# Performance work log

Measured on AMD Instinct MI355X. Metric: run time of the kernel, lower is better.

## Reference

```python
import math
import jax
import jax.numpy as jnp
import numpy as np

IMAGE_SIZE = 256
FOV_DEG = 60.0
NEAR, FAR = 0.01, 10.0
CHUNK = 128          # faces processed per scan step (bounds peak memory)
BIG_Z = 1e10         # 'infinite' depth for empty pixels


def _projection_matrix():
    f = 1.0 / math.tan(math.radians(FOV_DEG) / 2)
    return jnp.array([
        [f, 0.0, 0.0, 0.0],
        [0.0, f, 0.0, 0.0],
        [0.0, 0.0, (FAR + NEAR) / (NEAR - FAR), 2.0 * FAR * NEAR / (NEAR - FAR)],
        [0.0, 0.0, -1.0, 0.0],
    ], dtype=jnp.float32)


def _rasterize_mask(v_ndc, faces):
    """Coverage mask via edge-function triangle rasterization with a z-buffer.
    v_ndc: [V,3] ndc coords, faces: [F,3] int. Returns float [H,W] mask."""
    H = W = IMAGE_SIZE
    dt = v_ndc.dtype
    px = ((jnp.arange(W, dtype=dt) + 0.5) / W * 2.0 - 1.0)[None, None, :]  # [1,1,W]
    py = ((jnp.arange(H, dtype=dt) + 0.5) / H * 2.0 - 1.0)[None, :, None]  # [1,H,1]
    fchunks = faces.reshape(-1, CHUNK, 3)

    def body(carry, fc):
        zbuf, mask = carry
        tri = v_ndc[fc]  # [C,3,3]
        x0 = tri[:, 0, 0][:, None, None]; y0 = tri[:, 0, 1][:, None, None]; z0 = tri[:, 0, 2][:, None, None]
        x1 = tri[:, 1, 0][:, None, None]; y1 = tri[:, 1, 1][:, None, None]; z1 = tri[:, 1, 2][:, None, None]
        x2 = tri[:, 2, 0][:, None, None]; y2 = tri[:, 2, 1][:, None, None]; z2 = tri[:, 2, 2][:, None, None]
        # edge functions, [C,H,W]
        e0 = (x1 - x0) * (py - y0) - (y1 - y0) * (px - x0)
        e1 = (x2 - x1) * (py - y1) - (y2 - y1) * (px - x1)
        e2 = (x0 - x2) * (py - y2) - (y0 - y2) * (px - x2)
        inside = ((e0 >= 0) & (e1 >= 0) & (e2 >= 0)) | ((e0 <= 0) & (e1 <= 0) & (e2 <= 0))
        area = e0 + e1 + e2
        denom = jnp.where(jnp.abs(area) > 1e-12, area, 1.0)
        # barycentric-interpolated depth
        z = (e1 * z0 + e2 * z1 + e0 * z2) / denom
        zc = jnp.where(inside, z, BIG_Z)
        zbuf = jnp.minimum(zbuf, jnp.min(zc, axis=0))
        mask = jnp.maximum(mask, jnp.max(inside.astype(dt), axis=0))
        return (zbuf, mask), None

    zbuf0 = jnp.full((H, W), BIG_Z, dtype=dt)
    mask0 = jnp.zeros((H, W), dtype=dt)
    (_, mask), _ = jax.lax.scan(body, (zbuf0, mask0), fchunks)
    return mask


def setup_inputs() -> dict:
    key = jax.random.key(0)
    k1, k2, k3, k4 = jax.random.split(key, 4)
    B, V, F = 2, 4096, 4096
    verts = jax.random.normal(k1, (B, V, 3), dtype=jnp.float32)
    faces = jax.random.randint(k2, (B, F, 3), 0, V, dtype=jnp.int64 if jax.config.jax_enable_x64 else jnp.int32)
    R = jax.random.normal(k3, (B, 3, 3), dtype=jnp.float32)
    T = jax.random.normal(k4, (B, 3), dtype=jnp.float32)
    return {"verts": verts, "faces": faces, "R": R, "T": T}


def reference(verts, faces, R, T):
    proj = _projection_matrix()
    # world2cam: [R^T | -R^T t] with homogeneous bottom row, built batched
    Rt = jnp.swapaxes(R, -1, -2)                       # [B,3,3]
    t = -jnp.einsum('bij,bj->bi', Rt, T)               # [B,3]
    top = jnp.concatenate([Rt, t[..., None]], axis=-1)  # [B,3,4]
    bottom = jnp.broadcast_to(jnp.array([[0.0, 0.0, 0.0, 1.0]], dtype=verts.dtype), (R.shape[0], 1, 4))
    w2c = jnp.concatenate([top, bottom], axis=1)       # [B,4,4]
    VP = jnp.einsum('ij,bjk->bik', proj, w2c)          # [B,4,4]
    homo = jnp.concatenate([verts, jnp.ones_like(verts[..., :1])], axis=-1)  # [B,V,4]
    cam = jnp.einsum('bvk,bjk->bvj', homo, VP)         # verts_homo @ VP.T
    ndc = cam[..., :3] / jnp.maximum(cam[..., 3:], 1e-8)  # clamp(min=1e-8)
    mask = jax.vmap(_rasterize_mask)(ndc, faces)       # [B,H,W]
    return jnp.repeat(mask[..., None], 3, axis=-1)     # [B,H,W,3]
```

## Files before the change

kernel.cpp:

```cpp
#include <hip/hip_runtime.h>


#pragma clang fp contract(off)

#define HW      256
#define BATCH   2
#define VCOUNT  4096
#define FCOUNT  4096


__global__ __launch_bounds__(256)
void face_pack_kernel(const float* __restrict__ verts,
                      const int* __restrict__ faces,
                      const float* __restrict__ R,
                      const float* __restrict__ T,
                      float4* __restrict__ fpack)
{
#pragma clang fp contract(off)
    int gid = blockIdx.x * blockDim.x + threadIdx.x;
    if (gid >= BATCH * FCOUNT) return;
    int b = gid / FCOUNT;

    const float fproj = 1.7320508075688772f;

    const float* Rb = R + b * 9;
    const float* Tb = T + b * 3;

    float t0 = -((Rb[0*3+0]*Tb[0] + Rb[1*3+0]*Tb[1]) + Rb[2*3+0]*Tb[2]);
    float t1 = -((Rb[0*3+1]*Tb[0] + Rb[1*3+1]*Tb[1]) + Rb[2*3+1]*Tb[2]);
    float t2 = -((Rb[0*3+2]*Tb[0] + Rb[1*3+2]*Tb[1]) + Rb[2*3+2]*Tb[2]);

    float VP00 = fproj * Rb[0*3+0], VP01 = fproj * Rb[1*3+0],
          VP02 = fproj * Rb[2*3+0], VP03 = fproj * t0;
    float VP10 = fproj * Rb[0*3+1], VP11 = fproj * Rb[1*3+1],
          VP12 = fproj * Rb[2*3+1], VP13 = fproj * t1;
    float VP30 = -Rb[0*3+2], VP31 = -Rb[1*3+2],
          VP32 = -Rb[2*3+2], VP33 = -t2;

    const int* fp = faces + (size_t)gid * 3;
    float xs[3], ys[3];
#pragma unroll
    for (int j = 0; j < 3; ++j) {
        const float* vv = verts + ((size_t)b * VCOUNT + fp[j]) * 3;
        float vx = vv[0], vy = vv[1], vz = vv[2];
        float cx = ((vx*VP00 + vy*VP01) + vz*VP02) + VP03;
        float cy = ((vx*VP10 + vy*VP11) + vz*VP12) + VP13;
        float cw = ((vx*VP30 + vy*VP31) + vz*VP32) + VP33;
        float w = fmaxf(cw, 1e-8f);
        xs[j] = cx / w;
        ys[j] = cy / w;
    }

    float4* o = fpack + (size_t)gid * 3;
    o[0] = make_float4(xs[0], ys[0], xs[1], ys[1]);
    o[1] = make_float4(xs[2], ys[2], xs[1] - xs[0], ys[1] - ys[0]);
    o[2] = make_float4(xs[2] - xs[1], ys[2] - ys[1], xs[0] - xs[2], ys[0] - ys[2]);
}

__global__ __launch_bounds__(256)
void raster_kernel(const float4* __restrict__ fpack,
                   float* __restrict__ out)
{
#pragma clang fp contract(off)
    int b    = blockIdx.y;
    int tile = blockIdx.x;
    int px_i = ((tile & 15) << 4) + (threadIdx.x & 15);
    int py_i = ((tile >> 4) << 4) + (threadIdx.x >> 4);

    float px = (((float)px_i + 0.5f) / 256.0f) * 2.0f - 1.0f;
    float py = (((float)py_i + 0.5f) / 256.0f) * 2.0f - 1.0f;

    const float4* fb = fpack + (size_t)b * FCOUNT * 3;

    bool covered = false;

    for (int f8 = 0; f8 < FCOUNT; f8 += 8) {
        if (__all((int)covered)) break;
#pragma unroll
        for (int k = 0; k < 8; ++k) {
            const float4* q = fb + (size_t)(f8 + k) * 3;
            float4 a = q[0];
            float4 c = q[1];
            float4 d = q[2];
            float e0 = c.z * (py - a.y) - c.w * (px - a.x);
            float e1 = d.x * (py - a.w) - d.y * (px - a.z);
            float e2 = d.z * (py - c.y) - d.w * (px - c.x);
            float mn = fminf(fminf(e0, e1), e2);
            float mx = fmaxf(fmaxf(e0, e1), e2);
            covered = covered || (mn >= 0.0f) || (mx <= 0.0f);
        }
    }

    float val = covered ? 1.0f : 0.0f;
    size_t o = ((size_t)(b * HW + py_i) * HW + px_i) * 3;
    out[o + 0] = val;
    out[o + 1] = val;
    out[o + 2] = val;
}

extern "C" void kernel_launch(void* const* d_in, const int* in_sizes, int n_in,
                              void* d_out, int out_size, void* d_ws, size_t ws_size,
                              hipStream_t stream) {
    const float* verts = (const float*)d_in[0];
    const int*   faces = (const int*)d_in[1];
    const float* R     = (const float*)d_in[2];
    const float* T     = (const float*)d_in[3];
    float*       out   = (float*)d_out;

    float4* fpack = (float4*)d_ws;

    int nf = BATCH * FCOUNT;
    face_pack_kernel<<<(nf + 255) / 256, 256, 0, stream>>>(verts, faces, R, T, fpack);

    dim3 grid(256, BATCH);
    raster_kernel<<<grid, 256, 0, stream>>>(fpack, out);
}
```

Baseline: 65.67 us.

## Add per-wave conservative bounding-box culling of faces before edge tests

Face packing now also writes edge line equations with an error margin. In the raster kernel, each wave of 64 lanes tests 64 faces in parallel against its 16x4 pixel rectangle. A face is dropped only when every pixel lies strictly on both the negative and positive side of its edges, so it cannot cover any of them. Surviving faces are then walked one by one from a ballot mask. This replaces checking every face for every pixel with a cheap wave-wide cull plus sparse exact tests, at the cost of extra memory traffic, serial ffs loops and an epsilon margin that must stay conservative.

```diff
diff --git a/kernel.cpp b/kernel.cpp
--- a/kernel.cpp
+++ b/kernel.cpp
@@ -7,6 +7,7 @@
 #define BATCH   2
 #define VCOUNT  4096
 #define FCOUNT  4096
+#define CULL_EPS 1.52587890625e-05f
 
 
 __global__ __launch_bounds__(256)
@@ -14,7 +15,8 @@
                       const int* __restrict__ faces,
                       const float* __restrict__ R,
                       const float* __restrict__ T,
-                      float4* __restrict__ fpack)
+                      float4* __restrict__ fpack,
+                      float4* __restrict__ fcull)
 {
 #pragma clang fp contract(off)
     int gid = blockIdx.x * blockDim.x + threadIdx.x;
@@ -51,34 +53,87 @@
         ys[j] = cy / w;
     }
 
+    float d01x = xs[1] - xs[0], d01y = ys[1] - ys[0];
+    float d12x = xs[2] - xs[1], d12y = ys[2] - ys[1];
+    float d20x = xs[0] - xs[2], d20y = ys[0] - ys[2];
+
     float4* o = fpack + (size_t)gid * 3;
     o[0] = make_float4(xs[0], ys[0], xs[1], ys[1]);
-    o[1] = make_float4(xs[2], ys[2], xs[1] - xs[0], ys[1] - ys[0]);
-    o[2] = make_float4(xs[2] - xs[1], ys[2] - ys[1], xs[0] - xs[2], ys[0] - ys[2]);
+    o[1] = make_float4(xs[2], ys[2], d01x, d01y);
+    o[2] = make_float4(d12x, d12y, d20x, d20y);
+
+    float4* c = fcull + (size_t)gid * 3;
+    c[0] = make_float4(d01x, -d01y, d01y*xs[0] - d01x*ys[0],
+                       CULL_EPS * (fabsf(d01x)*(1.0f+fabsf(ys[0]))
+                                 + fabsf(d01y)*(1.0f+fabsf(xs[0]))));
+    c[1] = make_float4(d12x, -d12y, d12y*xs[1] - d12x*ys[1],
+                       CULL_EPS * (fabsf(d12x)*(1.0f+fabsf(ys[1]))
+                                 + fabsf(d12y)*(1.0f+fabsf(xs[1]))));
+    c[2] = make_float4(d20x, -d20y, d20y*xs[2] - d20x*ys[2],
+                       CULL_EPS * (fabsf(d20x)*(1.0f+fabsf(ys[2]))
+                                 + fabsf(d20y)*(1.0f+fabsf(xs[2]))));
+}
+
+__device__ __forceinline__ void cull_edge(float4 c, float pxlo, float pxhi,
+                                          float pylo, float pyhi,
+                                          bool& killneg, bool& killpos)
+{
+    float yh = (c.x > 0.0f) ? pyhi : pylo;
+    float yl = (c.x > 0.0f) ? pylo : pyhi;
+    float xh = (c.y > 0.0f) ? pxhi : pxlo;
+    float xl = (c.y > 0.0f) ? pxlo : pxhi;
+    float hi = c.x * yh + c.y * xh + c.z;
+    float lo = c.x * yl + c.y * xl + c.z;
+    killneg = killneg || (hi < -c.w);
+    killpos = killpos || (lo >  c.w);
 }
 
 __global__ __launch_bounds__(256)
 void raster_kernel(const float4* __restrict__ fpack,
+                   const float4* __restrict__ fcull,
                    float* __restrict__ out)
 {
 #pragma clang fp contract(off)
     int b    = blockIdx.y;
     int tile = blockIdx.x;
-    int px_i = ((tile & 15) << 4) + (threadIdx.x & 15);
-    int py_i = ((tile >> 4) << 4) + (threadIdx.x >> 4);
+    int tx = (tile & 15) << 4;
+    int ty = (tile >> 4) << 4;
+    int px_i = tx + (threadIdx.x & 15);
+    int py_i = ty + (threadIdx.x >> 4);
 
     float px = (((float)px_i + 0.5f) / 256.0f) * 2.0f - 1.0f;
     float py = (((float)py_i + 0.5f) / 256.0f) * 2.0f - 1.0f;
 
+    int wave = threadIdx.x >> 6;
+    int lane = threadIdx.x & 63;
+    int ry   = ty + wave * 4;
+    float pxlo = (((float)tx        + 0.5f) / 256.0f) * 2.0f - 1.0f;
+    float pxhi = (((float)(tx + 15) + 0.5f) / 256.0f) * 2.0f - 1.0f;
+    float pylo = (((float)ry        + 0.5f) / 256.0f) * 2.0f - 1.0f;
+    float pyhi = (((float)(ry + 3)  + 0.5f) / 256.0f) * 2.0f - 1.0f;
+
     const float4* fb = fpack + (size_t)b * FCOUNT * 3;
+    const float4* cb = fcull + (size_t)b * FCOUNT * 3;
 
     bool covered = false;
 
-    for (int f8 = 0; f8 < FCOUNT; f8 += 8) {
+    for (int g = 0; g < FCOUNT; g += 64) {
         if (__all((int)covered)) break;
-#pragma unroll
-        for (int k = 0; k < 8; ++k) {
-            const float4* q = fb + (size_t)(f8 + k) * 3;
+
+        const float4* cr = cb + (size_t)(g + lane) * 3;
+        float4 c0 = cr[0], c1 = cr[1], c2 = cr[2];
+        bool killneg = false, killpos = false;
+        cull_edge(c0, pxlo, pxhi, pylo, pyhi, killneg, killpos);
+        cull_edge(c1, pxlo, pxhi, pylo, pyhi, killneg, killpos);
+        cull_edge(c2, pxlo, pxhi, pylo, pyhi, killneg, killpos);
+        bool skip = killneg && killpos;
+
+        unsigned long long m = __ballot((int)!skip);
+        while (m) {
+            if (__all((int)covered)) break;
+            int k = __ffsll(m) - 1;
+            m &= m - 1;
+            const float4* q = fb + (size_t)(g + k) * 3;
             float4 a = q[0];
             float4 c = q[1];
             float4 d = q[2];
@@ -108,10 +163,12 @@
     float*       out   = (float*)d_out;
 
     float4* fpack = (float4*)d_ws;
+    float4* fcull = fpack + (size_t)BATCH * FCOUNT * 3;
 
     int nf = BATCH * FCOUNT;
-    face_pack_kernel<<<(nf + 255) / 256, 256, 0, stream>>>(verts, faces, R, T, fpack);
+    face_pack_kernel<<<(nf + 255) / 256, 256, 0, stream>>>(verts, faces, R, T,
+                                                           fpack, fcull);
 
     dim3 grid(256, BATCH);
-    raster_kernel<<<grid, 256, 0, stream>>>(fpack, out);
+    raster_kernel<<<grid, 256, 0, stream>>>(fpack, fcull, out);
 }
```

Result: faster. 63.64 us (-3.1%).

## Fuse face projection into raster kernel with per-tile conservative triangle culling

Applied to the files above, without the earlier changes.

Removes the separate face-pack kernel. Each 16x16 tile block now projects faces itself in chunks of 1024 and culls triangles that cannot cover the tile using a conservative edge-bound test. Survivors are compacted into shared memory with an atomic counter before the per-pixel edge tests run. This is meant to cut the per-pixel face loop and one launch, at the cost of every block redundantly projecting all faces and a larger shared-memory footprint, which may lower occupancy.

```diff
diff --git a/kernel.cpp b/kernel.cpp
--- a/kernel.cpp
+++ b/kernel.cpp
@@ -7,29 +7,41 @@
 #define BATCH   2
 #define VCOUNT  4096
 #define FCOUNT  4096
-
+#define CHUNK   1024
+#define CULL_EPS 1.52587890625e-05f
 
 __global__ __launch_bounds__(256)
-void face_pack_kernel(const float* __restrict__ verts,
-                      const int* __restrict__ faces,
-                      const float* __restrict__ R,
-                      const float* __restrict__ T,
-                      float4* __restrict__ fpack)
+void fused_raster_kernel(const float* __restrict__ verts,
+                         const int* __restrict__ faces,
+                         const float* __restrict__ R,
+                         const float* __restrict__ T,
+                         float* __restrict__ out)
 {
 #pragma clang fp contract(off)
-    int gid = blockIdx.x * blockDim.x + threadIdx.x;
-    if (gid >= BATCH * FCOUNT) return;
-    int b = gid / FCOUNT;
+    __shared__ float4 slist[CHUNK * 3];
+    __shared__ int scount;
+
+    int b    = blockIdx.y;
+    int tile = blockIdx.x;
+    int tid  = threadIdx.x;
+    int tx = (tile & 15) << 4;
+    int ty = (tile >> 4) << 4;
+    int px_i = tx + (tid & 15);
+    int py_i = ty + (tid >> 4);
+
+    float px = (((float)px_i + 0.5f) / 256.0f) * 2.0f - 1.0f;
+    float py = (((float)py_i + 0.5f) / 256.0f) * 2.0f - 1.0f;
+    float pxlo = (((float)tx        + 0.5f) / 256.0f) * 2.0f - 1.0f;
+    float pxhi = (((float)(tx + 15) + 0.5f) / 256.0f) * 2.0f - 1.0f;
+    float pylo = (((float)ty        + 0.5f) / 256.0f) * 2.0f - 1.0f;
+    float pyhi = (((float)(ty + 15) + 0.5f) / 256.0f) * 2.0f - 1.0f;
 
     const float fproj = 1.7320508075688772f;
-
     const float* Rb = R + b * 9;
     const float* Tb = T + b * 3;
-
     float t0 = -((Rb[0*3+0]*Tb[0] + Rb[1*3+0]*Tb[1]) + Rb[2*3+0]*Tb[2]);
     float t1 = -((Rb[0*3+1]*Tb[0] + Rb[1*3+1]*Tb[1]) + Rb[2*3+1]*Tb[2]);
     float t2 = -((Rb[0*3+2]*Tb[0] + Rb[1*3+2]*Tb[1]) + Rb[2*3+2]*Tb[2]);
-
     float VP00 = fproj * Rb[0*3+0], VP01 = fproj * Rb[1*3+0],
           VP02 = fproj * Rb[2*3+0], VP03 = fproj * t0;
     float VP10 = fproj * Rb[0*3+1], VP11 = fproj * Rb[1*3+1],
@@ -37,57 +49,81 @@
     float VP30 = -Rb[0*3+2], VP31 = -Rb[1*3+2],
           VP32 = -Rb[2*3+2], VP33 = -t2;
 
-    const int* fp = faces + (size_t)gid * 3;
-    float xs[3], ys[3];
-#pragma unroll
-    for (int j = 0; j < 3; ++j) {
-        const float* vv = verts + ((size_t)b * VCOUNT + fp[j]) * 3;
-        float vx = vv[0], vy = vv[1], vz = vv[2];
-        float cx = ((vx*VP00 + vy*VP01) + vz*VP02) + VP03;
-        float cy = ((vx*VP10 + vy*VP11) + vz*VP12) + VP13;
-        float cw = ((vx*VP30 + vy*VP31) + vz*VP32) + VP33;
-        float w = fmaxf(cw, 1e-8f);
-        xs[j] = cx / w;
-        ys[j] = cy / w;
-    }
-
-    float4* o = fpack + (size_t)gid * 3;
-    o[0] = make_float4(xs[0], ys[0], xs[1], ys[1]);
-    o[1] = make_float4(xs[2], ys[2], xs[1] - xs[0], ys[1] - ys[0]);
-    o[2] = make_float4(xs[2] - xs[1], ys[2] - ys[1], xs[0] - xs[2], ys[0] - ys[2]);
-}
-
-__global__ __launch_bounds__(256)
-void raster_kernel(const float4* __restrict__ fpack,
-                   float* __restrict__ out)
-{
-#pragma clang fp contract(off)
-    int b    = blockIdx.y;
-    int tile = blockIdx.x;
-    int px_i = ((tile & 15) << 4) + (threadIdx.x & 15);
-    int py_i = ((tile >> 4) << 4) + (threadIdx.x >> 4);
-
-    float px = (((float)px_i + 0.5f) / 256.0f) * 2.0f - 1.0f;
-    float py = (((float)py_i + 0.5f) / 256.0f) * 2.0f - 1.0f;
-
-    const float4* fb = fpack + (size_t)b * FCOUNT * 3;
+    const float* vb = verts + (size_t)b * VCOUNT * 3;
+    const int*   fb = faces + (size_t)b * FCOUNT * 3;
 
     bool covered = false;
 
-    for (int f8 = 0; f8 < FCOUNT; f8 += 8) {
-        if (__all((int)covered)) break;
+    for (int c0 = 0; c0 < FCOUNT; c0 += CHUNK) {
+        if (__syncthreads_and((int)covered)) break;
+        if (tid == 0) scount = 0;
+        __syncthreads();
+
+        for (int r = 0; r < CHUNK / 256; ++r) {
+            int fi = c0 + r * 256 + tid;
+            const int* fp = fb + (size_t)fi * 3;
+            int vi[3] = { fp[0], fp[1], fp[2] };
+            float xs[3], ys[3];
 #pragma unroll
-        for (int k = 0; k < 8; ++k) {
-            const float4* q = fb + (size_t)(f8 + k) * 3;
-            float4 a = q[0];
-            float4 c = q[1];
-            float4 d = q[2];
-            float e0 = c.z * (py - a.y) - c.w * (px - a.x);
-            float e1 = d.x * (py - a.w) - d.y * (px - a.z);
-            float e2 = d.z * (py - c.y) - d.w * (px - c.x);
-            float mn = fminf(fminf(e0, e1), e2);
-            float mx = fmaxf(fmaxf(e0, e1), e2);
-            covered = covered || (mn >= 0.0f) || (mx <= 0.0f);
+            for (int j = 0; j < 3; ++j) {
+                const float* vv = vb + (size_t)vi[j] * 3;
+                float vx = vv[0], vy = vv[1], vz = vv[2];
+                float cx = ((vx*VP00 + vy*VP01) + vz*VP02) + VP03;
+                float cy = ((vx*VP10 + vy*VP11) + vz*VP12) + VP13;
+                float cw = ((vx*VP30 + vy*VP31) + vz*VP32) + VP33;
+                float w = fmaxf(cw, 1e-8f);
+                xs[j] = cx / w;
+                ys[j] = cy / w;
+            }
+            float d01x = xs[1] - xs[0], d01y = ys[1] - ys[0];
+            float d12x = xs[2] - xs[1], d12y = ys[2] - ys[1];
+            float d20x = xs[0] - xs[2], d20y = ys[0] - ys[2];
+
+            bool killneg = false, killpos = false;
+            {
+                float A[3] = { d01x, d12x, d20x };
+                float B[3] = { -d01y, -d12y, -d20y };
+                float xa[3] = { xs[0], xs[1], xs[2] };
+                float ya[3] = { ys[0], ys[1], ys[2] };
+#pragma unroll
+                for (int e = 0; e < 3; ++e) {
+                    float C = (-B[e]) * xa[e] - A[e] * ya[e];
+                    float err = CULL_EPS * (fabsf(A[e]) * (1.0f + fabsf(ya[e]))
+                                          + fabsf(B[e]) * (1.0f + fabsf(xa[e])));
+                    float yh = (A[e] > 0.0f) ? pyhi : pylo;
+                    float yl = (A[e] > 0.0f) ? pylo : pyhi;
+                    float xh = (B[e] > 0.0f) ? pxhi : pxlo;
+                    float xl = (B[e] > 0.0f) ? pxlo : pxhi;
+                    float hi = A[e] * yh + B[e] * xh + C;
+                    float lo = A[e] * yl + B[e] * xl + C;
+                    killneg = killneg || (hi < -err);
+                    killpos = killpos || (lo >  err);
+                }
+            }
+            if (!(killneg && killpos)) {
+                int idx = atomicAdd(&scount, 1);
+                slist[idx*3 + 0] = make_float4(xs[0], ys[0], xs[1], ys[1]);
+                slist[idx*3 + 1] = make_float4(xs[2], ys[2], d01x, d01y);
+                slist[idx*3 + 2] = make_float4(d12x, d12y, d20x, d20y);
+            }
+        }
+        __syncthreads();
+
+        int n = scount;
+        for (int f8 = 0; f8 < n; f8 += 8) {
+            if (__all((int)covered)) break;
+            int fe = (f8 + 8 < n) ? f8 + 8 : n;
+            for (int f = f8; f < fe; ++f) {
+                float4 a = slist[f*3 + 0];
+                float4 c = slist[f*3 + 1];
+                float4 d = slist[f*3 + 2];
+                float e0 = c.z * (py - a.y) - c.w * (px - a.x);
+                float e1 = d.x * (py - a.w) - d.y * (px - a.z);
+                float e2 = d.z * (py - c.y) - d.w * (px - c.x);
+                float mn = fminf(fminf(e0, e1), e2);
+                float mx = fmaxf(fmaxf(e0, e1), e2);
+                covered = covered || (mn >= 0.0f) || (mx <= 0.0f);
+            }
         }
     }
 
@@ -107,11 +143,6 @@
     const float* T     = (const float*)d_in[3];
     float*       out   = (float*)d_out;
 
-    float4* fpack = (float4*)d_ws;
-
-    int nf = BATCH * FCOUNT;
-    face_pack_kernel<<<(nf + 255) / 256, 256, 0, stream>>>(verts, faces, R, T, fpack);
-
     dim3 grid(256, BATCH);
-    raster_kernel<<<grid, 256, 0, stream>>>(fpack, out);
+    fused_raster_kernel<<<grid, 256, 0, stream>>>(verts, faces, R, T, out);
 }
```

New measurement: 67.13 us. 2.2% more time.

## Cull faces per wave against the pixel-rectangle bounds before per-pixel edge tests

Applied to the files above, without the earlier changes.

Each wave loads 64 faces cooperatively, one per lane, and tests each face's three edge functions against the corners of the wave's 16x4 pixel rectangle, using a conservative epsilon. Faces whose edges rule out both orientations are skipped. Surviving faces are broadcast with shuffles and tested per pixel. The face buffer shrinks to six floats per face, with edge deltas recomputed in the raster kernel. This trades serialized ballot and shuffle iteration for far fewer edge evaluations, and it depends on the epsilon being conservative enough to keep exact coverage.

```diff
diff --git a/kernel.cpp b/kernel.cpp
--- a/kernel.cpp
+++ b/kernel.cpp
@@ -7,14 +7,15 @@
 #define BATCH   2
 #define VCOUNT  4096
 #define FCOUNT  4096
-
+#define CULL_EPS 1.52587890625e-05f
 
 __global__ __launch_bounds__(256)
 void face_pack_kernel(const float* __restrict__ verts,
                       const int* __restrict__ faces,
                       const float* __restrict__ R,
                       const float* __restrict__ T,
-                      float4* __restrict__ fpack)
+                      float4* __restrict__ fxy4,
+                      float2* __restrict__ fxy2)
 {
 #pragma clang fp contract(off)
     int gid = blockIdx.x * blockDim.x + threadIdx.x;
@@ -51,40 +52,87 @@
         ys[j] = cy / w;
     }
 
-    float4* o = fpack + (size_t)gid * 3;
-    o[0] = make_float4(xs[0], ys[0], xs[1], ys[1]);
-    o[1] = make_float4(xs[2], ys[2], xs[1] - xs[0], ys[1] - ys[0]);
-    o[2] = make_float4(xs[2] - xs[1], ys[2] - ys[1], xs[0] - xs[2], ys[0] - ys[2]);
+    fxy4[gid] = make_float4(xs[0], ys[0], xs[1], ys[1]);
+    fxy2[gid] = make_float2(xs[2], ys[2]);
 }
 
 __global__ __launch_bounds__(256)
-void raster_kernel(const float4* __restrict__ fpack,
+void raster_kernel(const float4* __restrict__ fxy4,
+                   const float2* __restrict__ fxy2,
                    float* __restrict__ out)
 {
 #pragma clang fp contract(off)
     int b    = blockIdx.y;
     int tile = blockIdx.x;
-    int px_i = ((tile & 15) << 4) + (threadIdx.x & 15);
-    int py_i = ((tile >> 4) << 4) + (threadIdx.x >> 4);
+    int tx = (tile & 15) << 4;
+    int ty = (tile >> 4) << 4;
+    int px_i = tx + (threadIdx.x & 15);
+    int py_i = ty + (threadIdx.x >> 4);
 
     float px = (((float)px_i + 0.5f) / 256.0f) * 2.0f - 1.0f;
     float py = (((float)py_i + 0.5f) / 256.0f) * 2.0f - 1.0f;
 
-    const float4* fb = fpack + (size_t)b * FCOUNT * 3;
+    int wave = threadIdx.x >> 6;
+    int lane = threadIdx.x & 63;
+    int ry   = ty + wave * 4;
+    float pxlo = (((float)tx        + 0.5f) / 256.0f) * 2.0f - 1.0f;
+    float pxhi = (((float)(tx + 15) + 0.5f) / 256.0f) * 2.0f - 1.0f;
+    float pylo = (((float)ry        + 0.5f) / 256.0f) * 2.0f - 1.0f;
+    float pyhi = (((float)(ry + 3)  + 0.5f) / 256.0f) * 2.0f - 1.0f;
+
+    const float4* f4 = fxy4 + (size_t)b * FCOUNT;
+    const float2* f2 = fxy2 + (size_t)b * FCOUNT;
 
     bool covered = false;
 
-    for (int f8 = 0; f8 < FCOUNT; f8 += 8) {
+    for (int g = 0; g < FCOUNT; g += 64) {
         if (__all((int)covered)) break;
+
+        float4 q0 = f4[g + lane];
+        float2 q1 = f2[g + lane];
+        float x0 = q0.x, y0 = q0.y, x1 = q0.z, y1 = q0.w;
+        float x2 = q1.x, y2 = q1.y;
+        float d01x = x1 - x0, d01y = y1 - y0;
+        float d12x = x2 - x1, d12y = y2 - y1;
+        float d20x = x0 - x2, d20y = y0 - y2;
+
+        bool killneg = false, killpos = false;
+        {
+            float A[3]  = { d01x, d12x, d20x };
+            float Bc[3] = { -d01y, -d12y, -d20y };
+            float xa[3] = { x0, x1, x2 };
+            float ya[3] = { y0, y1, y2 };
 #pragma unroll
-        for (int k = 0; k < 8; ++k) {
-            const float4* q = fb + (size_t)(f8 + k) * 3;
-            float4 a = q[0];
-            float4 c = q[1];
-            float4 d = q[2];
-            float e0 = c.z * (py - a.y) - c.w * (px - a.x);
-            float e1 = d.x * (py - a.w) - d.y * (px - a.z);
-            float e2 = d.z * (py - c.y) - d.w * (px - c.x);
+            for (int e = 0; e < 3; ++e) {
+                float C = (-Bc[e]) * xa[e] - A[e] * ya[e];
+                float err = CULL_EPS * (fabsf(A[e])  * (1.0f + fabsf(ya[e]))
+                                      + fabsf(Bc[e]) * (1.0f + fabsf(xa[e])));
+                float yh = (A[e]  > 0.0f) ? pyhi : pylo;
+                float yl = (A[e]  > 0.0f) ? pylo : pyhi;
+                float xh = (Bc[e] > 0.0f) ? pxhi : pxlo;
+                float xl = (Bc[e] > 0.0f) ? pxlo : pxhi;
+                float hi = A[e] * yh + Bc[e] * xh + C;
+                float lo = A[e] * yl + Bc[e] * xl + C;
+                killneg = killneg || (hi < -err);
+                killpos = killpos || (lo >  err);
+            }
+        }
+        bool skip = killneg && killpos;
+
+        unsigned long long m = __ballot((int)!skip);
+        while (m) {
+            if (__all((int)covered)) break;
+            int k = __ffsll((long long)m) - 1;
+            m &= m - 1;
+            float bx0 = __shfl(x0, k), by0 = __shfl(y0, k);
+            float bx1 = __shfl(x1, k), by1 = __shfl(y1, k);
+            float bx2 = __shfl(x2, k), by2 = __shfl(y2, k);
+            float bd01x = bx1 - bx0, bd01y = by1 - by0;
+            float bd12x = bx2 - bx1, bd12y = by2 - by1;
+            float bd20x = bx0 - bx2, bd20y = by0 - by2;
+            float e0 = bd01x * (py - by0) - bd01y * (px - bx0);
+            float e1 = bd12x * (py - by1) - bd12y * (px - bx1);
+            float e2 = bd20x * (py - by2) - bd20y * (px - bx2);
             float mn = fminf(fminf(e0, e1), e2);
             float mx = fmaxf(fmaxf(e0, e1), e2);
             covered = covered || (mn >= 0.0f) || (mx <= 0.0f);
@@ -107,11 +155,13 @@
     const float* T     = (const float*)d_in[3];
     float*       out   = (float*)d_out;
 
-    float4* fpack = (float4*)d_ws;
+    float4* fxy4 = (float4*)d_ws;
+    float2* fxy2 = (float2*)(fxy4 + BATCH * FCOUNT);
 
     int nf = BATCH * FCOUNT;
-    face_pack_kernel<<<(nf + 255) / 256, 256, 0, stream>>>(verts, faces, R, T, fpack);
+    face_pack_kernel<<<(nf + 255) / 256, 256, 0, stream>>>(verts, faces, R, T,
+                                                           fxy4, fxy2);
 
     dim3 grid(256, BATCH);
-    raster_kernel<<<grid, 256, 0, stream>>>(fpack, out);
+    raster_kernel<<<grid, 256, 0, stream>>>(fxy4, fxy2, out);
 }
```

After: 63.59 us. -3.2%, faster.
